# Kernel optimization log

Measured on AMD Instinct MI355X. Metric: run time of the kernel, lower is better.

Reference implementation:

```python
import jax, jax.numpy as jnp
import numpy as np

S, D, H, KV, HD = 2048, 4096, 32, 8, 128
N_REP = H // KV
THETA = 50000.0
EPS = 1e-6

# Precompute RoPE tables (constant, matches precompute_freqs_cis sliced to seq_len)
_freqs = 1.0 / THETA ** (np.arange(0, HD, 2)[: HD // 2].astype(np.float32) / HD)
_ang = np.outer(np.arange(S), _freqs).astype(np.float32)  # [S, HD//2]
COS = jnp.asarray(np.cos(_ang))
SIN = jnp.asarray(np.sin(_ang))


def _rope(x):
    # x: [S, nh, HD]; treat last dim as HD//2 complex pairs, multiply by e^{i*ang}
    xr = x.astype(jnp.float32).reshape(S, x.shape[1], HD // 2, 2)
    x0, x1 = xr[..., 0], xr[..., 1]
    c = COS[:, None, :]
    s = SIN[:, None, :]
    o0 = x0 * c - x1 * s
    o1 = x0 * s + x1 * c
    return jnp.stack((o0, o1), axis=-1).reshape(S, x.shape[1], HD)


def setup_inputs() -> dict:
    key = jax.random.key(0)
    k1, k2, k3, k4, k5 = jax.random.split(key, 5)
    w_scale = 0.02
    return {
        "hidden": jax.random.normal(k1, (S, D), dtype=jnp.float32),
        "norm_w": jnp.ones((D,), dtype=jnp.float32),
        "wq": jax.random.normal(k2, (H * HD, D), dtype=jnp.float32) * w_scale,
        "wk": jax.random.normal(k3, (KV * HD, D), dtype=jnp.float32) * w_scale,
        "wv": jax.random.normal(k4, (KV * HD, D), dtype=jnp.float32) * w_scale,
        "wo": jax.random.normal(k5, (D, D), dtype=jnp.float32) * w_scale,
    }


def reference(hidden, norm_w, wq, wk, wv, wo):
    # RMSNorm (per token)
    x = hidden.astype(jnp.float32)
    h = x * jax.lax.rsqrt(jnp.mean(x * x, axis=-1, keepdims=True) + EPS) * norm_w

    # QKV projections (eqx.nn.Linear: y = W @ x, no bias)
    q = (h @ wq.T).reshape(S, H, HD)
    k = (h @ wk.T).reshape(S, KV, HD)
    v = (h @ wv.T).reshape(S, KV, HD)

    # RoPE in fp32 (apply_rotary_emb with dtype=float32)
    q = _rope(q)
    k = _rope(k)

    # GQA: repeat kv heads to match query heads
    k = jnp.repeat(k[:, :, None, :], N_REP, axis=2).reshape(S, H, HD)
    v = jnp.repeat(v[:, :, None, :], N_REP, axis=2).reshape(S, H, HD)

    # Causal attention (full score matrix + softmax, as in the original)
    scores = jnp.einsum("shd,thd->hst", q, k) / jnp.sqrt(jnp.float32(HD))
    mask = jnp.triu(jnp.full((S, S), float("-inf"), dtype=scores.dtype), k=1)
    probs = jax.nn.softmax(scores + mask, axis=-1)
    attn = jnp.einsum("hst,thd->shd", probs, v).reshape(S, H * HD)

    # Output projection
    return attn @ wo.T
```

## Files before the change

### kernel.cpp

```cpp
#include <hip/hip_runtime.h>
#include <stdint.h>
#include <stddef.h>

#define AS1 __attribute__((address_space(1)))
#define AS3 __attribute__((address_space(3)))

typedef short short8 __attribute__((ext_vector_type(8)));
typedef float v4f    __attribute__((ext_vector_type(4)));
typedef unsigned short us4 __attribute__((ext_vector_type(4)));

constexpr int S_  = 2048;
constexpr int D_  = 4096;
constexpr int H_  = 32;
constexpr int KV_ = 8;
constexpr int HD_ = 128;
constexpr int NQKV_ = H_*HD_ + 2*KV_*HD_;
constexpr float SCALE_L2E = 0.12751744154070513f;
constexpr float NLOG2T_64 = -0.24390063241307518f;

__device__ __forceinline__ unsigned short f2bf(float f){
  union { float f; unsigned u; } v; v.f = f;
  unsigned r = v.u + 0x7FFFu + ((v.u >> 16) & 1u);
  return (unsigned short)(r >> 16);
}
__device__ __forceinline__ float bf2f(unsigned short h){
  union { unsigned u; float f; } v; v.u = ((unsigned)h) << 16; return v.f;
}

__device__ __forceinline__ void gl_lds16(const unsigned short* g, unsigned short* l){
  __builtin_amdgcn_global_load_lds((AS1 unsigned int*)(uintptr_t)g,
                                   (AS3 unsigned int*)l, 16, 0, 0);
}

__global__ __launch_bounds__(256) void rmsnorm_k(const float* __restrict__ hidden,
                                                 const float* __restrict__ w,
                                                 unsigned short* __restrict__ out){
  const int s = blockIdx.x, tid = threadIdx.x;
  const float4* row = (const float4*)(hidden + (size_t)s * D_);
  float4 v[4];
  float ss = 0.f;
  #pragma unroll
  for (int i = 0; i < 4; i++){
    float4 t = row[tid + 256*i]; v[i] = t;
    ss += t.x*t.x + t.y*t.y + t.z*t.z + t.w*t.w;
  }
  #pragma unroll
  for (int off = 32; off >= 1; off >>= 1) ss += __shfl_xor(ss, off, 64);
  __shared__ float wsum[4];
  if ((tid & 63) == 0) wsum[tid >> 6] = ss;
  __syncthreads();
  const float total = wsum[0] + wsum[1] + wsum[2] + wsum[3];
  const float r = rsqrtf(total * (1.0f / D_) + 1e-6f);
  const float4* w4 = (const float4*)w;
  us4* o = (us4*)(out + (size_t)s * D_);
  #pragma unroll
  for (int i = 0; i < 4; i++){
    float4 t = v[i], ww = w4[tid + 256*i];
    us4 p;
    p[0] = f2bf(t.x * r * ww.x); p[1] = f2bf(t.y * r * ww.y);
    p[2] = f2bf(t.z * r * ww.z); p[3] = f2bf(t.w * r * ww.w);
    o[tid + 256*i] = p;
  }
}

__global__ __launch_bounds__(256) void cast_k(const float* __restrict__ src,
                                              unsigned short* __restrict__ dst, int n4){
  const int i = blockIdx.x * 256 + threadIdx.x;
  if (i >= n4) return;
  float4 t = ((const float4*)src)[i];
  us4 p;
  p[0] = f2bf(t.x); p[1] = f2bf(t.y); p[2] = f2bf(t.z); p[3] = f2bf(t.w);
  ((us4*)dst)[i] = p;
}

__global__ __launch_bounds__(256) void gemm_bt(const unsigned short* __restrict__ A,
                                               const unsigned short* __restrict__ B,
                                               void* __restrict__ Cp,
                                               int K, int ldc, int f32out){
  __shared__ __align__(16) unsigned short sA[128*32];
  __shared__ __align__(16) unsigned short sB[128*32];
  const int tid = threadIdx.x;
  const int wave = tid >> 6, lane = tid & 63, l15 = lane & 15, quad = lane >> 4;
  const int m0 = blockIdx.y * 128, n0 = blockIdx.x * 128;
  const int wm = wave & 1, wn = wave >> 1;

  v4f acc[4][4];
  #pragma unroll
  for (int i = 0; i < 4; i++)
    #pragma unroll
    for (int j = 0; j < 4; j++) acc[i][j] = (v4f){0.f,0.f,0.f,0.f};

  const int arow = tid >> 2, acol = (tid & 3) * 8;
  const unsigned short* gA = A + (size_t)(m0 + arow) * K + acol;
  const unsigned short* gB = B + (size_t)(n0 + arow) * K + acol;
  unsigned short* lA = sA + wave * 512;
  unsigned short* lB = sB + wave * 512;

  for (int kt = 0; kt < K; kt += 32){
    gl_lds16(gA,                 lA);
    gl_lds16(gA + (size_t)64*K,  lA + 2048);
    gl_lds16(gB,                 lB);
    gl_lds16(gB + (size_t)64*K,  lB + 2048);
    gA += 32; gB += 32;
    __syncthreads();

    short8 af[4], bfr[4];
    #pragma unroll
    for (int mt = 0; mt < 4; mt++)
      af[mt] = *(const short8*)(sA + (wm*64 + mt*16 + l15)*32 + quad*8);
    #pragma unroll
    for (int nt = 0; nt < 4; nt++)
      bfr[nt] = *(const short8*)(sB + (wn*64 + nt*16 + l15)*32 + quad*8);
    #pragma unroll
    for (int mt = 0; mt < 4; mt++)
      #pragma unroll
      for (int nt = 0; nt < 4; nt++)
        acc[mt][nt] = __builtin_amdgcn_mfma_f32_16x16x32_bf16(af[mt], bfr[nt], acc[mt][nt], 0, 0, 0);
    __syncthreads();
  }

  if (f32out){
    float* Cf = (float*)Cp;
    #pragma unroll
    for (int mt = 0; mt < 4; mt++)
      #pragma unroll
      for (int r = 0; r < 4; r++){
        const size_t row = (size_t)(m0 + wm*64 + mt*16 + quad*4 + r);
        float* crow = Cf + row * ldc + n0 + wn*64 + l15;
        #pragma unroll
        for (int nt = 0; nt < 4; nt++) crow[nt*16] = acc[mt][nt][r];
      }
  } else {
    unsigned short* Cb = (unsigned short*)Cp;
    #pragma unroll
    for (int mt = 0; mt < 4; mt++)
      #pragma unroll
      for (int r = 0; r < 4; r++){
        const size_t row = (size_t)(m0 + wm*64 + mt*16 + quad*4 + r);
        unsigned short* crow = Cb + row * ldc + n0 + wn*64 + l15;
        #pragma unroll
        for (int nt = 0; nt < 4; nt++) crow[nt*16] = f2bf(acc[mt][nt][r]);
      }
  }
}

__global__ __launch_bounds__(256) void rope_q_k(const unsigned short* __restrict__ qkv,
                                                unsigned short* __restrict__ qa){
  const int idx = blockIdx.x * 256 + threadIdx.x;
  const int j = idx & 63, h = (idx >> 6) & (H_-1), s = idx >> 11;
  const unsigned pair = *(const unsigned*)(qkv + (size_t)s*NQKV_ + h*HD_ + 2*j);
  const float x0 = bf2f((unsigned short)(pair & 0xffffu));
  const float x1 = bf2f((unsigned short)(pair >> 16));
  const float ang = (float)s * exp2f((float)j * NLOG2T_64);
  const float c = __cosf(ang), sn = __sinf(ang);
  const unsigned o = (unsigned)f2bf(x0*c - x1*sn) | ((unsigned)f2bf(x0*sn + x1*c) << 16);
  *(unsigned*)(qa + ((size_t)h*S_ + s)*HD_ + 2*j) = o;
}

__global__ __launch_bounds__(256) void rope_kk(const unsigned short* __restrict__ qkv,
                                               unsigned short* __restrict__ ka){
  const int idx = blockIdx.x * 256 + threadIdx.x;
  const int j = idx & 63, kv = (idx >> 6) & (KV_-1), s = idx >> 9;
  const unsigned pair = *(const unsigned*)(qkv + (size_t)s*NQKV_ + H_*HD_ + kv*HD_ + 2*j);
  const float x0 = bf2f((unsigned short)(pair & 0xffffu));
  const float x1 = bf2f((unsigned short)(pair >> 16));
  const float ang = (float)s * exp2f((float)j * NLOG2T_64);
  const float c = __cosf(ang), sn = __sinf(ang);
  const unsigned o = (unsigned)f2bf(x0*c - x1*sn) | ((unsigned)f2bf(x0*sn + x1*c) << 16);
  *(unsigned*)(ka + ((size_t)kv*S_ + s)*HD_ + 2*j) = o;
}

__global__ __launch_bounds__(256) void vtrans_k(const unsigned short* __restrict__ qkv,
                                                unsigned short* __restrict__ vt){
  const int idx = blockIdx.x * 256 + threadIdx.x;
  const int s = idx & (S_-1), d = (idx >> 11) & (HD_-1), kv = idx >> 18;
  vt[idx] = qkv[(size_t)s*NQKV_ + (H_+KV_)*HD_ + kv*HD_ + d];
}

__device__ __forceinline__ void stage_kv(const unsigned short* __restrict__ ka,
                                         const unsigned short* __restrict__ vt,
                                         unsigned short* sKbuf, unsigned short* sVbuf,
                                         int hk, int t0, int wave, int lane){
  const int l15 = lane & 15, quad = lane >> 4;
  #pragma unroll
  for (int j = 0; j < 4; j++){
    const int c = wave*4 + j;
    const int kt = c >> 2, kk = c & 3;
    gl_lds16(ka + (size_t)(hk*S_ + t0 + kt*16 + l15)*HD_ + kk*32 + quad*8,
             sKbuf + c*512);
  }
  #pragma unroll
  for (int j = 0; j < 4; j++){
    const int c = wave*4 + j;
    const int nt = c >> 1, kk2 = c & 1;
    gl_lds16(vt + (size_t)(hk*HD_ + nt*16 + l15)*S_ + t0 + kk2*32 + quad*8,
             sVbuf + c*512);
  }
}

__global__ __launch_bounds__(256, 2) void attn_k(const unsigned short* __restrict__ qa,
                                                 const unsigned short* __restrict__ ka,
                                                 const unsigned short* __restrict__ vt,
                                                 unsigned short* __restrict__ out){
  const int h = blockIdx.x, qb = blockIdx.y;
  const int tid = threadIdx.x, wave = tid >> 6, lane = tid & 63;
  const int l15 = lane & 15, quad = lane >> 4;
  const int hk = h >> 2;
  const int qr0 = qb * 128 + wave * 32;

  __shared__ __align__(16) unsigned short sK[2][8192];
  __shared__ __align__(16) unsigned short sV[2][8192];
  __shared__ __align__(16) unsigned short sP[4][2048];
  unsigned short* pl = &sP[wave][0];

  short8 qf[2][4];
  #pragma unroll
  for (int qt = 0; qt < 2; qt++)
    #pragma unroll
    for (int kk = 0; kk < 4; kk++)
      qf[qt][kk] = *(const short8*)(qa + (size_t)(h*S_ + qr0 + qt*16 + l15)*HD_ + kk*32 + quad*8);

  v4f O[2][8];
  #pragma unroll
  for (int qt = 0; qt < 2; qt++)
    #pragma unroll
    for (int nt = 0; nt < 8; nt++) O[qt][nt] = (v4f){0.f,0.f,0.f,0.f};
  float mrow[2][4], lrow[2][4];
  #pragma unroll
  for (int qt = 0; qt < 2; qt++)
    #pragma unroll
    for (int r = 0; r < 4; r++){ mrow[qt][r] = -1e30f; lrow[qt][r] = 0.f; }

  const int nblk = 2*qb + 2;

  stage_kv(ka, vt, sK[0], sV[0], hk, 0, wave, lane);
  __syncthreads();

  for (int b = 0; b < nblk; b++){
    const int t0 = b * 64;
    const int cur = b & 1;
    if (b + 1 < nblk)
      stage_kv(ka, vt, sK[cur^1], sV[cur^1], hk, t0 + 64, wave, lane);

    const unsigned short* Kb = &sK[cur][0];
    v4f sc[2][4];
    #pragma unroll
    for (int qt = 0; qt < 2; qt++)
      #pragma unroll
      for (int kt = 0; kt < 4; kt++) sc[qt][kt] = (v4f){0.f,0.f,0.f,0.f};
    #pragma unroll
    for (int kt = 0; kt < 4; kt++)
      #pragma unroll
      for (int kk = 0; kk < 4; kk++){
        const short8 kf = *(const short8*)(Kb + (kt*4 + kk)*512 + lane*8);
        sc[0][kt] = __builtin_amdgcn_mfma_f32_16x16x32_bf16(qf[0][kk], kf, sc[0][kt], 0, 0, 0);
        sc[1][kt] = __builtin_amdgcn_mfma_f32_16x16x32_bf16(qf[1][kk], kf, sc[1][kt], 0, 0, 0);
      }

    #pragma unroll
    for (int qt = 0; qt < 2; qt++){
      const int rowq = qr0 + qt*16 + quad*4;
      const bool needMask = (t0 + 63 > qr0 + qt*16);
      float alpha[4];
      #pragma unroll
      for (int r = 0; r < 4; r++){
        float a0 = sc[qt][0][r] * SCALE_L2E;
        float a1 = sc[qt][1][r] * SCALE_L2E;
        float a2 = sc[qt][2][r] * SCALE_L2E;
        float a3 = sc[qt][3][r] * SCALE_L2E;
        if (needMask){
          const int row = rowq + r;
          if (t0      + l15 > row) a0 = -1e30f;
          if (t0 + 16 + l15 > row) a1 = -1e30f;
          if (t0 + 32 + l15 > row) a2 = -1e30f;
          if (t0 + 48 + l15 > row) a3 = -1e30f;
        }
        float mx = fmaxf(fmaxf(a0, a1), fmaxf(a2, a3));
        #pragma unroll
        for (int off = 1; off < 16; off <<= 1) mx = fmaxf(mx, __shfl_xor(mx, off, 16));
        const float mnew = fmaxf(mrow[qt][r], mx);
        const float al = exp2f(mrow[qt][r] - mnew);
        const float e0 = exp2f(a0 - mnew);
        const float e1 = exp2f(a1 - mnew);
        const float e2 = exp2f(a2 - mnew);
        const float e3 = exp2f(a3 - mnew);
        float rs = (e0 + e1) + (e2 + e3);
        #pragma unroll
        for (int off = 1; off < 16; off <<= 1) rs += __shfl_xor(rs, off, 16);
        lrow[qt][r] = lrow[qt][r]*al + rs;
        mrow[qt][r] = mnew;
        alpha[r] = al;
        pl[(qt*2 + 0)*512 + (0 + (l15>>3))*128 + (quad*4+r)*8 + (l15&7)] = f2bf(e0);
        pl[(qt*2 + 0)*512 + (2 + (l15>>3))*128 + (quad*4+r)*8 + (l15&7)] = f2bf(e1);
        pl[(qt*2 + 1)*512 + (0 + (l15>>3))*128 + (quad*4+r)*8 + (l15&7)] = f2bf(e2);
        pl[(qt*2 + 1)*512 + (2 + (l15>>3))*128 + (quad*4+r)*8 + (l15&7)] = f2bf(e3);
      }
      #pragma unroll
      for (int nt = 0; nt < 8; nt++)
        #pragma unroll
        for (int r = 0; r < 4; r++) O[qt][nt][r] *= alpha[r];
    }

    __builtin_amdgcn_s_waitcnt(0xC07F);
    short8 pf[2][2];
    #pragma unroll
    for (int qt = 0; qt < 2; qt++)
      #pragma unroll
      for (int kk2 = 0; kk2 < 2; kk2++)
        pf[qt][kk2] = *(const short8*)(pl + (qt*2 + kk2)*512 + lane*8);

    const unsigned short* Vb = &sV[cur][0];
    #pragma unroll
    for (int nt = 0; nt < 8; nt++)
      #pragma unroll
      for (int kk2 = 0; kk2 < 2; kk2++){
        const short8 vf = *(const short8*)(Vb + (nt*2 + kk2)*512 + lane*8);
        O[0][nt] = __builtin_amdgcn_mfma_f32_16x16x32_bf16(pf[0][kk2], vf, O[0][nt], 0, 0, 0);
        O[1][nt] = __builtin_amdgcn_mfma_f32_16x16x32_bf16(pf[1][kk2], vf, O[1][nt], 0, 0, 0);
      }

    __syncthreads();
  }

  #pragma unroll
  for (int qt = 0; qt < 2; qt++){
    float inv[4];
    #pragma unroll
    for (int r = 0; r < 4; r++) inv[r] = 1.0f / lrow[qt][r];
    #pragma unroll
    for (int nt = 0; nt < 8; nt++)
      #pragma unroll
      for (int r = 0; r < 4; r++)
        out[(size_t)(qr0 + qt*16 + quad*4 + r)*D_ + h*HD_ + nt*16 + l15] = f2bf(O[qt][nt][r] * inv[r]);
  }
}

extern "C" void kernel_launch(void* const* d_in, const int* in_sizes, int n_in,
                              void* d_out, int out_size, void* d_ws, size_t ws_size,
                              hipStream_t stream){
  (void)in_sizes; (void)n_in; (void)out_size; (void)ws_size;
  const float* hidden = (const float*)d_in[0];
  const float* norm_w = (const float*)d_in[1];
  const float* wq = (const float*)d_in[2];
  const float* wk = (const float*)d_in[3];
  const float* wv = (const float*)d_in[4];
  const float* wo = (const float*)d_in[5];

  char* ws = (char*)d_ws;
  unsigned short* h_bf  = (unsigned short*)(ws);
  unsigned short* wqkv  = (unsigned short*)(ws + (size_t)(16u) * 1048576u);
  unsigned short* qkv   = (unsigned short*)(ws + (size_t)(64u) * 1048576u);
  unsigned short* qa    = (unsigned short*)(ws + (size_t)(88u) * 1048576u);
  unsigned short* ka    = (unsigned short*)(ws + (size_t)(104u) * 1048576u);
  unsigned short* vt    = (unsigned short*)(ws + (size_t)(108u) * 1048576u);
  unsigned short* wo_bf = (unsigned short*)(ws + (size_t)(16u) * 1048576u);
  unsigned short* attnb = (unsigned short*)(ws + (size_t)(48u) * 1048576u);

  rmsnorm_k<<<S_, 256, 0, stream>>>(hidden, norm_w, h_bf);

  cast_k<<<(D_*D_/4)/256, 256, 0, stream>>>(wq, wqkv, D_*D_/4);
  cast_k<<<(KV_*HD_*D_/4)/256, 256, 0, stream>>>(wk, wqkv + (size_t)H_*HD_*D_, KV_*HD_*D_/4);
  cast_k<<<(KV_*HD_*D_/4)/256, 256, 0, stream>>>(wv, wqkv + (size_t)(H_+KV_)*HD_*D_, KV_*HD_*D_/4);

  gemm_bt<<<dim3(NQKV_/128, S_/128), 256, 0, stream>>>(h_bf, wqkv, qkv, D_, NQKV_, 0);

  rope_q_k<<<(S_*H_*64)/256, 256, 0, stream>>>(qkv, qa);
  rope_kk <<<(S_*KV_*64)/256, 256, 0, stream>>>(qkv, ka);
  vtrans_k<<<(KV_*HD_*S_)/256, 256, 0, stream>>>(qkv, vt);

  cast_k<<<(D_*D_/4)/256, 256, 0, stream>>>(wo, wo_bf, D_*D_/4);

  attn_k<<<dim3(H_, S_/128), 256, 0, stream>>>(qa, ka, vt, attnb);

  gemm_bt<<<dim3(D_/128, S_/128), 256, 0, stream>>>(attnb, wo_bf, d_out, D_, D_, 1);
}
```

Before: 626.2 us.

## Pair causal attention tiles per block and compute row sums via MFMA

The attention kernel now gives each block two 64-row query tiles, one near the end and one near the start of the sequence (p and 31-p), so every block handles the same number of key blocks and causal load imbalance goes away. Each wave now owns 16 query rows instead of 32, which halves per-wave register and LDS use. The softmax scale is folded into Q during RoPE, and the row-sum reduction uses an MFMA against a ones vector instead of shuffles. The trade-off is less K/V reuse per staged block, since only 64 query rows share each staged tile instead of 128, and the row sums are now taken from bf16-rounded probabilities.

New measurement: 556.8 us. 1.12x faster.

```diff
diff --git a/kernel.cpp b/kernel.cpp
--- a/kernel.cpp
+++ b/kernel.cpp
@@ -153,7 +153,8 @@
   const float x1 = bf2f((unsigned short)(pair >> 16));
   const float ang = (float)s * exp2f((float)j * NLOG2T_64);
   const float c = __cosf(ang), sn = __sinf(ang);
-  const unsigned o = (unsigned)f2bf(x0*c - x1*sn) | ((unsigned)f2bf(x0*sn + x1*c) << 16);
+  const unsigned o = (unsigned)f2bf((x0*c - x1*sn) * SCALE_L2E)
+                   | ((unsigned)f2bf((x0*sn + x1*c) * SCALE_L2E) << 16);
   *(unsigned*)(qa + ((size_t)h*S_ + s)*HD_ + 2*j) = o;
 }
 
@@ -202,136 +203,141 @@
                                                  const unsigned short* __restrict__ ka,
                                                  const unsigned short* __restrict__ vt,
                                                  unsigned short* __restrict__ out){
-  const int h = blockIdx.x, qb = blockIdx.y;
+  const int h = blockIdx.x, p = blockIdx.y;
   const int tid = threadIdx.x, wave = tid >> 6, lane = tid & 63;
   const int l15 = lane & 15, quad = lane >> 4;
   const int hk = h >> 2;
-  const int qr0 = qb * 128 + wave * 32;
+  const int nbB = 32 - p;
+  const int total = nbB + p + 1;
 
   __shared__ __align__(16) unsigned short sK[2][8192];
   __shared__ __align__(16) unsigned short sV[2][8192];
-  __shared__ __align__(16) unsigned short sP[4][2048];
+  __shared__ __align__(16) unsigned short sP[4][1024];
   unsigned short* pl = &sP[wave][0];
 
-  short8 qf[2][4];
-  #pragma unroll
-  for (int qt = 0; qt < 2; qt++)
-    #pragma unroll
-    for (int kk = 0; kk < 4; kk++)
-      qf[qt][kk] = *(const short8*)(qa + (size_t)(h*S_ + qr0 + qt*16 + l15)*HD_ + kk*32 + quad*8);
-
-  v4f O[2][8];
-  #pragma unroll
-  for (int qt = 0; qt < 2; qt++)
-    #pragma unroll
-    for (int nt = 0; nt < 8; nt++) O[qt][nt] = (v4f){0.f,0.f,0.f,0.f};
-  float mrow[2][4], lrow[2][4];
-  #pragma unroll
-  for (int qt = 0; qt < 2; qt++)
-    #pragma unroll
-    for (int r = 0; r < 4; r++){ mrow[qt][r] = -1e30f; lrow[qt][r] = 0.f; }
-
-  const int nblk = 2*qb + 2;
+  short8 ones;
+  #pragma unroll
+  for (int i = 0; i < 8; i++) ones[i] = (short)0x3F80;
+
+  int tile = 31 - p;
+  short8 qf[4];
+  {
+    const unsigned short* qb = qa + (size_t)(h*S_ + tile*64 + wave*16 + l15)*HD_ + quad*8;
+    #pragma unroll
+    for (int kk = 0; kk < 4; kk++) qf[kk] = *(const short8*)(qb + kk*32);
+  }
+
+  v4f O[8];
+  #pragma unroll
+  for (int nt = 0; nt < 8; nt++) O[nt] = (v4f){0.f,0.f,0.f,0.f};
+  float mrow[4], lrow[4];
+  #pragma unroll
+  for (int r = 0; r < 4; r++){ mrow[r] = -1e30f; lrow[r] = 0.f; }
 
   stage_kv(ka, vt, sK[0], sV[0], hk, 0, wave, lane);
   __syncthreads();
 
-  for (int b = 0; b < nblk; b++){
-    const int t0 = b * 64;
-    const int cur = b & 1;
-    if (b + 1 < nblk)
-      stage_kv(ka, vt, sK[cur^1], sV[cur^1], hk, t0 + 64, wave, lane);
+  for (int u = 0; u < total; ++u){
+    const int cur = u & 1;
+    if (u + 1 < total){
+      const int b2 = (u + 1 < nbB) ? u + 1 : u + 1 - nbB;
+      stage_kv(ka, vt, sK[cur^1], sV[cur^1], hk, b2*64, wave, lane);
+    }
 
     const unsigned short* Kb = &sK[cur][0];
-    v4f sc[2][4];
-    #pragma unroll
-    for (int qt = 0; qt < 2; qt++)
-      #pragma unroll
-      for (int kt = 0; kt < 4; kt++) sc[qt][kt] = (v4f){0.f,0.f,0.f,0.f};
+    v4f sc[4];
+    #pragma unroll
+    for (int kt = 0; kt < 4; kt++) sc[kt] = (v4f){0.f,0.f,0.f,0.f};
     #pragma unroll
     for (int kt = 0; kt < 4; kt++)
       #pragma unroll
       for (int kk = 0; kk < 4; kk++){
         const short8 kf = *(const short8*)(Kb + (kt*4 + kk)*512 + lane*8);
-        sc[0][kt] = __builtin_amdgcn_mfma_f32_16x16x32_bf16(qf[0][kk], kf, sc[0][kt], 0, 0, 0);
-        sc[1][kt] = __builtin_amdgcn_mfma_f32_16x16x32_bf16(qf[1][kk], kf, sc[1][kt], 0, 0, 0);
-      }
-
-    #pragma unroll
-    for (int qt = 0; qt < 2; qt++){
-      const int rowq = qr0 + qt*16 + quad*4;
-      const bool needMask = (t0 + 63 > qr0 + qt*16);
-      float alpha[4];
+        sc[kt] = __builtin_amdgcn_mfma_f32_16x16x32_bf16(qf[kk], kf, sc[kt], 0, 0, 0);
+      }
+
+    const bool diag = (u == nbB - 1) || (u == total - 1);
+    float alpha[4];
+    #pragma unroll
+    for (int r = 0; r < 4; r++){
+      float a0 = sc[0][r], a1 = sc[1][r], a2 = sc[2][r], a3 = sc[3][r];
+      if (diag){
+        const int rloc = wave*16 + quad*4 + r;
+        if (     l15 > rloc) a0 = -1e30f;
+        if (16 + l15 > rloc) a1 = -1e30f;
+        if (32 + l15 > rloc) a2 = -1e30f;
+        if (48 + l15 > rloc) a3 = -1e30f;
+      }
+      float mx = fmaxf(fmaxf(a0, a1), fmaxf(a2, a3));
+      #pragma unroll
+      for (int off = 1; off < 16; off <<= 1) mx = fmaxf(mx, __shfl_xor(mx, off, 16));
+      const float mnew = fmaxf(mrow[r], mx);
+      alpha[r] = exp2f(mrow[r] - mnew);
+      mrow[r] = mnew;
+      const float e0 = exp2f(a0 - mnew);
+      const float e1 = exp2f(a1 - mnew);
+      const float e2 = exp2f(a2 - mnew);
+      const float e3 = exp2f(a3 - mnew);
+      const int mr = (quad*4 + r)*8 + (l15 & 7);
+      const int hi = (l15 >> 3) * 128;
+      pl[      hi       + mr] = f2bf(e0);
+      pl[      hi + 256 + mr] = f2bf(e1);
+      pl[512 + hi       + mr] = f2bf(e2);
+      pl[512 + hi + 256 + mr] = f2bf(e3);
+    }
+    #pragma unroll
+    for (int nt = 0; nt < 8; nt++)
+      #pragma unroll
+      for (int r = 0; r < 4; r++) O[nt][r] *= alpha[r];
+
+    __builtin_amdgcn_s_waitcnt(0xC07F);
+    const short8 pf0 = *(const short8*)(pl + lane*8);
+    const short8 pf1 = *(const short8*)(pl + 512 + lane*8);
+
+    v4f rs = (v4f){0.f,0.f,0.f,0.f};
+    rs = __builtin_amdgcn_mfma_f32_16x16x32_bf16(pf0, ones, rs, 0, 0, 0);
+    rs = __builtin_amdgcn_mfma_f32_16x16x32_bf16(pf1, ones, rs, 0, 0, 0);
+
+    const unsigned short* Vb = &sV[cur][0];
+    #pragma unroll
+    for (int nt = 0; nt < 8; nt++){
+      const short8 vf0 = *(const short8*)(Vb + (nt*2    )*512 + lane*8);
+      const short8 vf1 = *(const short8*)(Vb + (nt*2 + 1)*512 + lane*8);
+      O[nt] = __builtin_amdgcn_mfma_f32_16x16x32_bf16(pf0, vf0, O[nt], 0, 0, 0);
+      O[nt] = __builtin_amdgcn_mfma_f32_16x16x32_bf16(pf1, vf1, O[nt], 0, 0, 0);
+    }
+    #pragma unroll
+    for (int r = 0; r < 4; r++) lrow[r] = lrow[r]*alpha[r] + rs[r];
+
+    __syncthreads();
+
+    if (u == nbB - 1){
       #pragma unroll
       for (int r = 0; r < 4; r++){
-        float a0 = sc[qt][0][r] * SCALE_L2E;
-        float a1 = sc[qt][1][r] * SCALE_L2E;
-        float a2 = sc[qt][2][r] * SCALE_L2E;
-        float a3 = sc[qt][3][r] * SCALE_L2E;
-        if (needMask){
-          const int row = rowq + r;
-          if (t0      + l15 > row) a0 = -1e30f;
-          if (t0 + 16 + l15 > row) a1 = -1e30f;
-          if (t0 + 32 + l15 > row) a2 = -1e30f;
-          if (t0 + 48 + l15 > row) a3 = -1e30f;
-        }
-        float mx = fmaxf(fmaxf(a0, a1), fmaxf(a2, a3));
+        const float inv = 1.0f / lrow[r];
+        const size_t row = (size_t)(tile*64 + wave*16 + quad*4 + r);
         #pragma unroll
-        for (int off = 1; off < 16; off <<= 1) mx = fmaxf(mx, __shfl_xor(mx, off, 16));
-        const float mnew = fmaxf(mrow[qt][r], mx);
-        const float al = exp2f(mrow[qt][r] - mnew);
-        const float e0 = exp2f(a0 - mnew);
-        const float e1 = exp2f(a1 - mnew);
-        const float e2 = exp2f(a2 - mnew);
-        const float e3 = exp2f(a3 - mnew);
-        float rs = (e0 + e1) + (e2 + e3);
-        #pragma unroll
-        for (int off = 1; off < 16; off <<= 1) rs += __shfl_xor(rs, off, 16);
-        lrow[qt][r] = lrow[qt][r]*al + rs;
-        mrow[qt][r] = mnew;
-        alpha[r] = al;
-        pl[(qt*2 + 0)*512 + (0 + (l15>>3))*128 + (quad*4+r)*8 + (l15&7)] = f2bf(e0);
-        pl[(qt*2 + 0)*512 + (2 + (l15>>3))*128 + (quad*4+r)*8 + (l15&7)] = f2bf(e1);
-        pl[(qt*2 + 1)*512 + (0 + (l15>>3))*128 + (quad*4+r)*8 + (l15&7)] = f2bf(e2);
-        pl[(qt*2 + 1)*512 + (2 + (l15>>3))*128 + (quad*4+r)*8 + (l15&7)] = f2bf(e3);
-      }
-      #pragma unroll
-      for (int nt = 0; nt < 8; nt++)
-        #pragma unroll
-        for (int r = 0; r < 4; r++) O[qt][nt][r] *= alpha[r];
+        for (int nt = 0; nt < 8; nt++)
+          out[row*D_ + h*HD_ + nt*16 + l15] = f2bf(O[nt][r] * inv);
+      }
+      tile = p;
+      const unsigned short* qb = qa + (size_t)(h*S_ + tile*64 + wave*16 + l15)*HD_ + quad*8;
+      #pragma unroll
+      for (int kk = 0; kk < 4; kk++) qf[kk] = *(const short8*)(qb + kk*32);
+      #pragma unroll
+      for (int nt = 0; nt < 8; nt++) O[nt] = (v4f){0.f,0.f,0.f,0.f};
+      #pragma unroll
+      for (int r = 0; r < 4; r++){ mrow[r] = -1e30f; lrow[r] = 0.f; }
     }
-
-    __builtin_amdgcn_s_waitcnt(0xC07F);
-    short8 pf[2][2];
-    #pragma unroll
-    for (int qt = 0; qt < 2; qt++)
-      #pragma unroll
-      for (int kk2 = 0; kk2 < 2; kk2++)
-        pf[qt][kk2] = *(const short8*)(pl + (qt*2 + kk2)*512 + lane*8);
-
-    const unsigned short* Vb = &sV[cur][0];
+  }
+
+  #pragma unroll
+  for (int r = 0; r < 4; r++){
+    const float inv = 1.0f / lrow[r];
+    const size_t row = (size_t)(tile*64 + wave*16 + quad*4 + r);
     #pragma unroll
     for (int nt = 0; nt < 8; nt++)
-      #pragma unroll
-      for (int kk2 = 0; kk2 < 2; kk2++){
-        const short8 vf = *(const short8*)(Vb + (nt*2 + kk2)*512 + lane*8);
-        O[0][nt] = __builtin_amdgcn_mfma_f32_16x16x32_bf16(pf[0][kk2], vf, O[0][nt], 0, 0, 0);
-        O[1][nt] = __builtin_amdgcn_mfma_f32_16x16x32_bf16(pf[1][kk2], vf, O[1][nt], 0, 0, 0);
-      }
-
-    __syncthreads();
-  }
-
-  #pragma unroll
-  for (int qt = 0; qt < 2; qt++){
-    float inv[4];
-    #pragma unroll
-    for (int r = 0; r < 4; r++) inv[r] = 1.0f / lrow[qt][r];
-    #pragma unroll
-    for (int nt = 0; nt < 8; nt++)
-      #pragma unroll
-      for (int r = 0; r < 4; r++)
-        out[(size_t)(qr0 + qt*16 + quad*4 + r)*D_ + h*HD_ + nt*16 + l15] = f2bf(O[qt][nt][r] * inv[r]);
+      out[row*D_ + h*HD_ + nt*16 + l15] = f2bf(O[nt][r] * inv);
   }
 }
 
@@ -370,7 +376,7 @@
 
   cast_k<<<(D_*D_/4)/256, 256, 0, stream>>>(wo, wo_bf, D_*D_/4);
 
-  attn_k<<<dim3(H_, S_/128), 256, 0, stream>>>(qa, ka, vt, attnb);
+  attn_k<<<dim3(H_, 16), 256, 0, stream>>>(qa, ka, vt, attnb);
 
   gemm_bt<<<dim3(D_/128, S_/128), 256, 0, stream>>>(attnb, wo_bf, d_out, D_, D_, 1);
 }
```
